# Optimization experiments

Hardware: AMD Instinct MI355X
Metric: run time of the kernel (lower is better)

## Reference

```python
import jax, jax.numpy as jnp
import numpy as np
import math

HIDDEN = 768
HEADS = 12
HEAD_DIM = HIDDEN // HEADS
B, T = 2, 2048


def setup_inputs() -> dict:
    key = jax.random.key(0)
    k1, k2, k3, k4, k5 = jax.random.split(key, 5)
    s = 0.02
    return {
        "x": jax.random.normal(k1, (B, T, HIDDEN), dtype=jnp.float32),
        "mask": jnp.ones((B, T), dtype=jnp.int32),
        "w_qkv": jax.random.normal(k2, (3 * HIDDEN, HIDDEN), dtype=jnp.float32) * s,
        "b_qkv": jnp.zeros((3 * HIDDEN,), dtype=jnp.float32),
        "w_out": jax.random.normal(k3, (HIDDEN, HIDDEN), dtype=jnp.float32) * s,
        "b_out": jnp.zeros((HIDDEN,), dtype=jnp.float32),
    }


def reference(x, mask, w_qkv, b_qkv, w_out, b_out):
    Bv, Tv, C = x.shape
    # torch Linear: y = x @ W.T + b
    qkv = jnp.einsum('btc,oc->bto', x, w_qkv) + b_qkv  # [B,T,3C]
    q, k, v = jnp.split(qkv, 3, axis=-1)
    def to_heads(t):
        return t.reshape(Bv, Tv, HEADS, HEAD_DIM).transpose(0, 2, 1, 3)  # [B,H,T,D]
    q, k, v = to_heads(q), to_heads(k), to_heads(v)
    scale = 1.0 / math.sqrt(HEAD_DIM)
    scores = jnp.einsum('bhqd,bhkd->bhqk', q, k) * scale  # [B,H,T,T]
    m = (mask[:, None, None, :] != 0)  # broadcast over heads and query dim
    scores = jnp.where(m, scores, -jnp.inf)
    probs = jax.nn.softmax(scores, axis=-1)
    # dropout is identity in eval mode
    ctx = jnp.einsum('bhqk,bhkd->bhqd', probs, v)  # [B,H,T,D]
    ctx = ctx.transpose(0, 2, 1, 3).reshape(Bv, Tv, C)
    return jnp.einsum('btc,oc->bto', ctx, w_out) + b_out
```

## Files before the change

kernel.cpp:

```cpp
#include <hip/hip_runtime.h>
#include <hip/hip_bf16.h>


typedef __bf16 bf16;
typedef __attribute__((ext_vector_type(4))) __bf16 bf16x4;
typedef __attribute__((ext_vector_type(8))) __bf16 bf16x8;
typedef __attribute__((ext_vector_type(4))) float f32x4;
typedef __attribute__((ext_vector_type(16))) float f32x16;
typedef __attribute__((ext_vector_type(4))) unsigned u32x4;

#define MFMA16(a, b, c) __builtin_amdgcn_mfma_f32_16x16x32_bf16((a), (b), (c), 0, 0, 0)
#define MFMA32(a, b, c) __builtin_amdgcn_mfma_f32_32x32x16_bf16((a), (b), (c), 0, 0, 0)

static constexpr int BB = 2;
static constexpr int TT = 2048;
static constexpr int CC = 768;
static constexpr int HH = 12;
static constexpr int DD = 64;

union U8 { u32x4 u; bf16x8 b; };

__device__ inline void gload16(const bf16* g, bf16* l) {
  __builtin_amdgcn_global_load_lds((const __attribute__((address_space(1))) void*)g,
                                   (__attribute__((address_space(3))) void*)l, 16, 0, 0);
}

__global__ __launch_bounds__(256) void cvt_all(const float* __restrict__ x,
                                               const float* __restrict__ wq,
                                               const float* __restrict__ wo,
                                               bf16* __restrict__ xb,
                                               bf16* __restrict__ wqb,
                                               bf16* __restrict__ wob) {
  const int CX = BB * TT * CC / 8, CQ = 3 * CC * CC / 8;
  int idx = blockIdx.x * 256 + threadIdx.x;
  const float* s;
  bf16* d;
  int off;
  if (idx < CX) { s = x; d = xb; off = idx; }
  else if (idx < CX + CQ) { s = wq; d = wqb; off = idx - CX; }
  else { s = wo; d = wob; off = idx - CX - CQ; }
  const float4* p = (const float4*)(s + (size_t)off * 8);
  float4 a = p[0], b = p[1];
  bf16x8 r;
  r[0] = (bf16)a.x; r[1] = (bf16)a.y; r[2] = (bf16)a.z; r[3] = (bf16)a.w;
  r[4] = (bf16)b.x; r[5] = (bf16)b.y; r[6] = (bf16)b.z; r[7] = (bf16)b.w;
  *(bf16x8*)(d + (size_t)off * 8) = r;
}

template <typename OT>
__global__ __launch_bounds__(256) void gemm_bt_bf16(const bf16* __restrict__ A,
                                                    const bf16* __restrict__ Bw,
                                                    const float* __restrict__ bias,
                                                    OT* __restrict__ Cmat,
                                                    int M, int N, int K,
                                                    float qs, int qcols) {
  __shared__ bf16 As[128 * 64];
  __shared__ bf16 Bs[128 * 64];
  const int tid = threadIdx.x;
  const int m0 = blockIdx.y * 128, n0 = blockIdx.x * 128;
  const int lane = tid & 63, w = tid >> 6;
  const int wm = (w >> 1) * 64, wn = (w & 1) * 64;
  const int lr = lane & 15;
  const int g4 = lane >> 4;
  const int srow8 = lane >> 3;
  const int scs = ((lane & 7) ^ srow8) * 8;
  f32x4 acc[4][4] = {};
  for (int k0 = 0; k0 < K; k0 += 64) {
    __syncthreads();
#pragma unroll
    for (int s = 0; s < 4; s++) {
      const int rowl = w * 32 + s * 8;
      gload16(A  + (size_t)(m0 + rowl + srow8) * K + k0 + scs, &As[rowl * 64]);
      gload16(Bw + (size_t)(n0 + rowl + srow8) * K + k0 + scs, &Bs[rowl * 64]);
    }
    __syncthreads();
#pragma unroll
    for (int ks = 0; ks < 2; ks++) {
      bf16x8 a[4], b[4];
#pragma unroll
      for (int i = 0; i < 4; i++)
        a[i] = *(const bf16x8*)&As[(wm + i * 16 + lr) * 64 + (((ks * 4 + g4) ^ (lr & 7)) * 8)];
#pragma unroll
      for (int j = 0; j < 4; j++)
        b[j] = *(const bf16x8*)&Bs[(wn + j * 16 + lr) * 64 + (((ks * 4 + g4) ^ (lr & 7)) * 8)];
#pragma unroll
      for (int i = 0; i < 4; i++)
#pragma unroll
        for (int j = 0; j < 4; j++)
          acc[i][j] = MFMA16(a[i], b[j], acc[i][j]);
    }
  }
#pragma unroll
  for (int i = 0; i < 4; i++) {
    const int rbase = m0 + wm + i * 16 + (lane >> 4) * 4;
#pragma unroll
    for (int j = 0; j < 4; j++) {
      const int cidx = n0 + wn + j * 16 + lr;
      const float bv = bias[cidx];
      const float sc = (cidx < qcols) ? qs : 1.0f;
#pragma unroll
      for (int r = 0; r < 4; r++) {
        float v = (acc[i][j][r] + bv) * sc;
        Cmat[(size_t)(rbase + r) * N + cidx] = (OT)v;
      }
    }
  }
}

template <int NS>
__global__ __launch_bounds__(256, 4) void attn_fwd(const bf16* __restrict__ qkv,
                                                   const int* __restrict__ mask,
                                                   bf16* __restrict__ po,
                                                   float* __restrict__ ml,
                                                   bf16* __restrict__ ctx) {
  __shared__ bf16 Ks[2][64 * 64];
  __shared__ bf16 Vt[2][64 * 64];
  const int tid = threadIdx.x, lane = tid & 63, w = tid >> 6;
  const int ln31 = lane & 31, hi = lane >> 5;
  const int cpx = 48 * NS;
  const int bid = blockIdx.x;
  const int wg = (bid & 7) * cpx + (bid >> 3);
  const int qb = wg & 15;
  const int t2 = wg >> 4;
  const int s = t2 % NS;
  const int bh = t2 / NS;
  const int h = bh % HH, b = bh / HH;
  const int q = qb * 128 + w * 32 + ln31;
  const size_t rs = 3 * CC;
  const float NEG = -1.0e30f;
  const int kt0 = s * (TT / NS), kt1 = kt0 + TT / NS;

  bf16x8 qreg[4];
  {
    const bf16* qp = qkv + (size_t)(b * TT + q) * rs + h * DD + hi * 8;
#pragma unroll
    for (int ds = 0; ds < 4; ds++) qreg[ds] = *(const bf16x8*)(qp + ds * 16);
  }

  const bf16* kbase = qkv + (size_t)(b * TT) * rs + CC + h * DD;
  const bf16* vbase = qkv + (size_t)(b * TT) * rs + 2 * CC + h * DD;

  const int krow = lane >> 3;
  const int klc0 = ((lane & 7) ^ (w & 7)) * 8;
  const int klc1 = ((lane & 7) ^ ((w + 4) & 7)) * 8;
  auto stage_k = [&](int buf, int kt) {
    gload16(kbase + (size_t)(kt + w * 8 + krow) * rs + klc0, &Ks[buf][(w * 8) * 64]);
    gload16(kbase + (size_t)(kt + 32 + w * 8 + krow) * rs + klc1, &Ks[buf][(32 + w * 8) * 64]);
  };

  const int vkey = tid >> 2;
  const int vd0 = (tid & 3) * 16;
  const int vpar = vkey & 1;
  const int vkp = vkey >> 1;
  bf16x8 vr0, vr1;
  int mv;
  auto load_v = [&](int kt) {
    const bf16* vp = vbase + (size_t)(kt + vkey) * rs + vd0;
    vr0 = ((const bf16x8*)vp)[0];
    vr1 = ((const bf16x8*)vp)[1];
    mv = mask[b * TT + kt + lane];
  };
  auto vt_put = [&](int buf, int d, unsigned val) {
    *(unsigned*)&Vt[buf][d * 64 + (((vkp >> 2) ^ ((d >> 3) & 7)) * 8) + (vkp & 3) * 2] = val;
  };
  auto write_v = [&](int buf) {
    U8 ua, ub; ua.b = vr0; ub.b = vr1;
    unsigned w0 = ua.u[0], w1 = ua.u[1], w2 = ua.u[2], w3 = ua.u[3];
    unsigned w4 = ub.u[0], w5 = ub.u[1], w6 = ub.u[2], w7 = ub.u[3];
    unsigned x0 = vpar ? w0 : w4, x1 = vpar ? w1 : w5;
    unsigned x2 = vpar ? w2 : w6, x3 = vpar ? w3 : w7;
    unsigned r0 = __shfl_xor(x0, 4), r1 = __shfl_xor(x1, 4);
    unsigned r2 = __shfl_xor(x2, 4), r3 = __shfl_xor(x3, 4);
    unsigned a0 = vpar ? r0 : w0, a1 = vpar ? r1 : w1;
    unsigned a2 = vpar ? r2 : w2, a3 = vpar ? r3 : w3;
    unsigned b0 = vpar ? w4 : r0, b1 = vpar ? w5 : r1;
    unsigned b2 = vpar ? w6 : r2, b3 = vpar ? w7 : r3;
    const int dbase = vd0 + vpar * 8;
    vt_put(buf, dbase + 0, (a0 & 0xffffu) | (b0 << 16));
    vt_put(buf, dbase + 1, (a0 >> 16) | (b0 & 0xffff0000u));
    vt_put(buf, dbase + 2, (a1 & 0xffffu) | (b1 << 16));
    vt_put(buf, dbase + 3, (a1 >> 16) | (b1 & 0xffff0000u));
    vt_put(buf, dbase + 4, (a2 & 0xffffu) | (b2 << 16));
    vt_put(buf, dbase + 5, (a2 >> 16) | (b2 & 0xffff0000u));
    vt_put(buf, dbase + 6, (a3 & 0xffffu) | (b3 << 16));
    vt_put(buf, dbase + 7, (a3 >> 16) | (b3 & 0xffff0000u));
  };

  stage_k(0, kt0);
  load_v(kt0);
  write_v(0);
  __syncthreads();
  int mvc = mv;

  f32x16 oacc0 = {}, oacc1 = {};
  float m = NEG, l = 0.f;
  const int rsw0 = (ln31 >> 3) & 7;
  const int rsw1 = ((32 + ln31) >> 3) & 7;

  int cur = 0;
  for (int kt = kt0; kt < kt1; kt += 64, cur ^= 1) {
    const bool more = kt + 64 < kt1;
    if (more) { stage_k(cur ^ 1, kt + 64); load_v(kt + 64); }

    f32x16 sa = {}, sb = {};
    __builtin_amdgcn_s_setprio(1);
#pragma unroll
    for (int ds = 0; ds < 4; ds++) {
      const int c0 = ds * 2 + hi;
      bf16x8 kfa = *(const bf16x8*)&Ks[cur][ln31 * 64 + ((c0 ^ rsw0) * 8)];
      sa = MFMA32(kfa, qreg[ds], sa);
      bf16x8 kfb = *(const bf16x8*)&Ks[cur][(32 + ln31) * 64 + ((c0 ^ rsw1) * 8)];
      sb = MFMA32(kfb, qreg[ds], sb);
    }
    __builtin_amdgcn_s_setprio(0);

    const unsigned long long bm = __ballot(mvc != 0);
    if (bm != ~0ull) {
#pragma unroll
      for (int r = 0; r < 16; r++) {
        const int key = (r & 3) + 8 * (r >> 2) + 4 * hi;
        if (!((bm >> key) & 1)) sa[r] = NEG;
        if (!((bm >> (key + 32)) & 1)) sb[r] = NEG;
      }
    }

    float mx = fmaxf(sa[0], sb[0]);
#pragma unroll
    for (int r = 1; r < 16; r++) mx = fmaxf(mx, fmaxf(sa[r], sb[r]));
    mx = fmaxf(mx, __shfl_xor(mx, 32));
    if (!__all(mx - m <= 8.f)) {
      const float al = exp2f(m - mx);
      l *= al;
#pragma unroll
      for (int r = 0; r < 16; r++) { oacc0[r] *= al; oacc1[r] *= al; }
      m = mx;
    }
    float rsum = 0.f;
#pragma unroll
    for (int r = 0; r < 16; r++) {
      sa[r] = exp2f(sa[r] - m); rsum += sa[r];
      sb[r] = exp2f(sb[r] - m); rsum += sb[r];
    }
    rsum += __shfl_xor(rsum, 32);
    l += rsum;

    unsigned pk[16];
#pragma unroll
    for (int i = 0; i < 8; i++) {
      asm("v_cvt_pk_bf16_f32 %0, %1, %2" : "=v"(pk[i]) : "v"(sa[2 * i]), "v"(sa[2 * i + 1]));
      asm("v_cvt_pk_bf16_f32 %0, %1, %2" : "=v"(pk[8 + i]) : "v"(sb[2 * i]), "v"(sb[2 * i + 1]));
    }
    asm volatile("v_permlane32_swap_b32 %0, %1" : "+v"(pk[0]), "+v"(pk[2]));
    asm volatile("v_permlane32_swap_b32 %0, %1" : "+v"(pk[1]), "+v"(pk[3]));
    asm volatile("v_permlane32_swap_b32 %0, %1" : "+v"(pk[4]), "+v"(pk[6]));
    asm volatile("v_permlane32_swap_b32 %0, %1" : "+v"(pk[5]), "+v"(pk[7]));
    asm volatile("v_permlane32_swap_b32 %0, %1" : "+v"(pk[8]), "+v"(pk[10]));
    asm volatile("v_permlane32_swap_b32 %0, %1" : "+v"(pk[9]), "+v"(pk[11]));
    asm volatile("v_permlane32_swap_b32 %0, %1" : "+v"(pk[12]), "+v"(pk[14]));
    asm volatile("v_permlane32_swap_b32 %0, %1" : "+v"(pk[13]), "+v"(pk[15]));

    __builtin_amdgcn_s_setprio(1);
#pragma unroll
    for (int ks = 0; ks < 4; ks++) {
      U8 uu;
      uu.u = (u32x4){pk[ks * 4 + 0], pk[ks * 4 + 1], pk[ks * 4 + 2], pk[ks * 4 + 3]};
      const bf16x8 pb = uu.b;
      const int c0 = ks * 2 + hi;
      bf16x8 vf0 = *(const bf16x8*)&Vt[cur][ln31 * 64 + ((c0 ^ rsw0) * 8)];
      oacc0 = MFMA32(vf0, pb, oacc0);
      bf16x8 vf1 = *(const bf16x8*)&Vt[cur][(32 + ln31) * 64 + ((c0 ^ rsw1) * 8)];
      oacc1 = MFMA32(vf1, pb, oacc1);
    }
    __builtin_amdgcn_s_setprio(0);

    if (more) write_v(cur ^ 1);
    __syncthreads();
    mvc = mv;
  }

  const float invl = l > 0.f ? 1.0f / l : 0.f;
  const size_t gr = (size_t)(b * TT + q);
  bf16* obase = (NS == 1) ? (ctx + gr * CC + h * DD)
                          : (po + (size_t)s * (BB * TT * CC) + gr * CC + h * DD);
#pragma unroll
  for (int g = 0; g < 4; g++) {
    bf16x4 o0, o1;
#pragma unroll
    for (int j = 0; j < 4; j++) {
      o0[j] = (bf16)(oacc0[4 * g + j] * invl);
      o1[j] = (bf16)(oacc1[4 * g + j] * invl);
    }
    *(bf16x4*)(obase + 8 * g + 4 * hi) = o0;
    *(bf16x4*)(obase + 32 + 8 * g + 4 * hi) = o1;
  }
  if (NS > 1 && hi == 0) {
    float2 v2 = {m, l};
    *(float2*)&ml[(((size_t)s * (BB * TT) + gr) * HH + h) * 2] = v2;
  }
}

template <int NS>
__global__ __launch_bounds__(256) void combine(const bf16* __restrict__ po,
                                               const float* __restrict__ ml,
                                               bf16* __restrict__ ctx) {
  const int idx = blockIdx.x * 256 + threadIdx.x;
  const int row = idx / 96;
  const int rem = idx - row * 96;
  const int h = rem >> 3, d8 = rem & 7;
  float ms[NS], ls[NS];
  float M = -1.0e30f;
#pragma unroll
  for (int s = 0; s < NS; s++) {
    const float2 p2 = *(const float2*)&ml[(((size_t)s * (BB * TT) + row) * HH + h) * 2];
    ms[s] = p2.x; ls[s] = p2.y;
    M = fmaxf(M, p2.x);
  }
  float wgt[NS], wsum = 0.f;
#pragma unroll
  for (int s = 0; s < NS; s++) { wgt[s] = ls[s] * exp2f(ms[s] - M); wsum += wgt[s]; }
  const float inv = wsum > 0.f ? 1.0f / wsum : 0.f;
  float acc[8] = {};
#pragma unroll
  for (int s = 0; s < NS; s++) {
    const float ws = wgt[s] * inv;
    const bf16x8 v = *(const bf16x8*)&po[(size_t)s * (BB * TT * CC) + (size_t)row * CC + h * 64 + d8 * 8];
#pragma unroll
    for (int j = 0; j < 8; j++) acc[j] += ws * (float)v[j];
  }
  bf16x8 o;
#pragma unroll
  for (int j = 0; j < 8; j++) o[j] = (bf16)acc[j];
  *(bf16x8*)&ctx[(size_t)row * CC + h * 64 + d8 * 8] = o;
}

extern "C" void kernel_launch(void* const* d_in, const int* in_sizes, int n_in,
                              void* d_out, int out_size, void* d_ws, size_t ws_size,
                              hipStream_t stream) {
  const float* x     = (const float*)d_in[0];
  const int*   mask  = (const int*)d_in[1];
  const float* w_qkv = (const float*)d_in[2];
  const float* b_qkv = (const float*)d_in[3];
  const float* w_out = (const float*)d_in[4];
  const float* b_out = (const float*)d_in[5];
  float* out = (float*)d_out;

  const int M = BB * TT;
  bf16* qkv = (bf16*)d_ws;
  bf16* xb  = qkv + (size_t)M * 3 * CC;
  bf16* ctx = xb;
  bf16* wob = xb + (size_t)M * CC;
  bf16* wqb = wob + (size_t)CC * CC;
  const size_t PO_OFF = (size_t)((M * 3 * CC) + (M * CC) + (CC * CC)) * 2;
  const size_t PER_SPLIT = (size_t)M * CC * 2 + (size_t)M * HH * 2 * 4;

  int NS = 1;
  if (ws_size >= PO_OFF + 4 * PER_SPLIT) NS = 4;
  else if (ws_size >= PO_OFF + 2 * PER_SPLIT) NS = 2;

  bf16* po = (bf16*)((char*)d_ws + PO_OFF);
  float* ml = (float*)((char*)d_ws + PO_OFF + (size_t)NS * M * CC * 2);

  const int nchunks = (BB * TT * CC + 3 * CC * CC + CC * CC) / 8;
  cvt_all<<<nchunks / 256, 256, 0, stream>>>(x, w_qkv, w_out, xb, wqb, wob);
  gemm_bt_bf16<bf16><<<dim3(3 * CC / 128, M / 128), 256, 0, stream>>>(
      xb, wqb, b_qkv, qkv, M, 3 * CC, CC, 0.125f * 1.44269504f, CC);
  if (NS == 4) {
    attn_fwd<4><<<dim3(384 * 4), 256, 0, stream>>>(qkv, mask, po, ml, ctx);
    combine<4><<<dim3(M * HH * 8 / 256), 256, 0, stream>>>(po, ml, ctx);
  } else if (NS == 2) {
    attn_fwd<2><<<dim3(384 * 2), 256, 0, stream>>>(qkv, mask, po, ml, ctx);
    combine<2><<<dim3(M * HH * 8 / 256), 256, 0, stream>>>(po, ml, ctx);
  } else {
    attn_fwd<1><<<dim3(384), 256, 0, stream>>>(qkv, mask, po, ml, ctx);
  }
  gemm_bt_bf16<float><<<dim3(CC / 128, M / 128), 256, 0, stream>>>(
      ctx, wob, b_out, out, M, CC, CC, 1.0f, 0);
}
```

Measured before the change: 128.7 us.

## Split softmax exp and PV MFMA into halves to overlap VALU with MFMA

```diff
diff --git a/kernel.cpp b/kernel.cpp
--- a/kernel.cpp
+++ b/kernel.cpp
@@ -108,11 +108,11 @@
 }
 
 template <int NS>
-__global__ __launch_bounds__(256, 4) void attn_fwd(const bf16* __restrict__ qkv,
-                                                   const int* __restrict__ mask,
-                                                   bf16* __restrict__ po,
-                                                   float* __restrict__ ml,
-                                                   bf16* __restrict__ ctx) {
+__global__ __launch_bounds__(256) void attn_fwd(const bf16* __restrict__ qkv,
+                                                const int* __restrict__ mask,
+                                                bf16* __restrict__ po,
+                                                float* __restrict__ ml,
+                                                bf16* __restrict__ ctx) {
   __shared__ bf16 Ks[2][64 * 64];
   __shared__ bf16 Vt[2][64 * 64];
   const int tid = threadIdx.x, lane = tid & 63, w = tid >> 6;
@@ -128,7 +128,8 @@
   const int q = qb * 128 + w * 32 + ln31;
   const size_t rs = 3 * CC;
   const float NEG = -1.0e30f;
-  const int kt0 = s * (TT / NS), kt1 = kt0 + TT / NS;
+  const int kt0 = s * (TT / NS);
+  const int NT = (TT / NS) / 64;
 
   bf16x8 qreg[4];
   {
@@ -143,23 +144,19 @@
   const int krow = lane >> 3;
   const int klc0 = ((lane & 7) ^ (w & 7)) * 8;
   const int klc1 = ((lane & 7) ^ ((w + 4) & 7)) * 8;
-  auto stage_k = [&](int buf, int kt) {
-    gload16(kbase + (size_t)(kt + w * 8 + krow) * rs + klc0, &Ks[buf][(w * 8) * 64]);
-    gload16(kbase + (size_t)(kt + 32 + w * 8 + krow) * rs + klc1, &Ks[buf][(32 + w * 8) * 64]);
-  };
+  const bf16* kptA = kbase + (size_t)(kt0 + w * 8 + krow) * rs + klc0;
+  const bf16* kptB = kbase + (size_t)(kt0 + 32 + w * 8 + krow) * rs + klc1;
 
   const int vkey = tid >> 2;
   const int vd0 = (tid & 3) * 16;
   const int vpar = vkey & 1;
   const int vkp = vkey >> 1;
+  const bf16* vptr = vbase + (size_t)(kt0 + vkey) * rs + vd0;
+  const int* mptr = mask + b * TT + kt0 + lane;
+  const size_t stride = (size_t)64 * rs;
+
   bf16x8 vr0, vr1;
   int mv;
-  auto load_v = [&](int kt) {
-    const bf16* vp = vbase + (size_t)(kt + vkey) * rs + vd0;
-    vr0 = ((const bf16x8*)vp)[0];
-    vr1 = ((const bf16x8*)vp)[1];
-    mv = mask[b * TT + kt + lane];
-  };
   auto vt_put = [&](int buf, int d, unsigned val) {
     *(unsigned*)&Vt[buf][d * 64 + (((vkp >> 2) ^ ((d >> 3) & 7)) * 8) + (vkp & 3) * 2] = val;
   };
@@ -186,9 +183,13 @@
     vt_put(buf, dbase + 7, (a3 >> 16) | (b3 & 0xffff0000u));
   };
 
-  stage_k(0, kt0);
-  load_v(kt0);
+  gload16(kptA, &Ks[0][(w * 8) * 64]);
+  gload16(kptB, &Ks[0][(32 + w * 8) * 64]);
+  vr0 = ((const bf16x8*)vptr)[0];
+  vr1 = ((const bf16x8*)vptr)[1];
+  mv = *mptr;
   write_v(0);
+  kptA += stride; kptB += stride; vptr += stride; mptr += 64;
   __syncthreads();
   int mvc = mv;
 
@@ -198,9 +199,16 @@
   const int rsw1 = ((32 + ln31) >> 3) & 7;
 
   int cur = 0;
-  for (int kt = kt0; kt < kt1; kt += 64, cur ^= 1) {
-    const bool more = kt + 64 < kt1;
-    if (more) { stage_k(cur ^ 1, kt + 64); load_v(kt + 64); }
+  for (int it = 0; it < NT; ++it, cur ^= 1) {
+    const bool more = (it + 1 < NT);
+    if (more) {
+      gload16(kptA, &Ks[cur ^ 1][(w * 8) * 64]);
+      gload16(kptB, &Ks[cur ^ 1][(32 + w * 8) * 64]);
+      vr0 = ((const bf16x8*)vptr)[0];
+      vr1 = ((const bf16x8*)vptr)[1];
+      mv = *mptr;
+      kptA += stride; kptB += stride; vptr += stride; mptr += 64;
+    }
 
     f32x16 sa = {}, sb = {};
     __builtin_amdgcn_s_setprio(1);
@@ -224,9 +232,12 @@
       }
     }
 
-    float mx = fmaxf(sa[0], sb[0]);
-#pragma unroll
-    for (int r = 1; r < 16; r++) mx = fmaxf(mx, fmaxf(sa[r], sb[r]));
+    float t[8];
+#pragma unroll
+    for (int i = 0; i < 8; i++)
+      t[i] = fmaxf(fmaxf(sa[2 * i], sa[2 * i + 1]), fmaxf(sb[2 * i], sb[2 * i + 1]));
+    float mx = fmaxf(fmaxf(fmaxf(t[0], t[1]), fmaxf(t[2], t[3])),
+                     fmaxf(fmaxf(t[4], t[5]), fmaxf(t[6], t[7])));
     mx = fmaxf(mx, __shfl_xor(mx, 32));
     if (!__all(mx - m <= 8.f)) {
       const float al = exp2f(m - mx);
@@ -235,43 +246,55 @@
       for (int r = 0; r < 16; r++) { oacc0[r] *= al; oacc1[r] *= al; }
       m = mx;
     }
+
     float rsum = 0.f;
-#pragma unroll
-    for (int r = 0; r < 16; r++) {
-      sa[r] = exp2f(sa[r] - m); rsum += sa[r];
-      sb[r] = exp2f(sb[r] - m); rsum += sb[r];
-    }
-    rsum += __shfl_xor(rsum, 32);
-    l += rsum;
-
-    unsigned pk[16];
-#pragma unroll
-    for (int i = 0; i < 8; i++) {
+    unsigned pk[8];
+#pragma unroll
+    for (int r = 0; r < 16; r++) { sa[r] = exp2f(sa[r] - m); rsum += sa[r]; }
+#pragma unroll
+    for (int i = 0; i < 8; i++)
       asm("v_cvt_pk_bf16_f32 %0, %1, %2" : "=v"(pk[i]) : "v"(sa[2 * i]), "v"(sa[2 * i + 1]));
-      asm("v_cvt_pk_bf16_f32 %0, %1, %2" : "=v"(pk[8 + i]) : "v"(sb[2 * i]), "v"(sb[2 * i + 1]));
-    }
     asm volatile("v_permlane32_swap_b32 %0, %1" : "+v"(pk[0]), "+v"(pk[2]));
     asm volatile("v_permlane32_swap_b32 %0, %1" : "+v"(pk[1]), "+v"(pk[3]));
     asm volatile("v_permlane32_swap_b32 %0, %1" : "+v"(pk[4]), "+v"(pk[6]));
     asm volatile("v_permlane32_swap_b32 %0, %1" : "+v"(pk[5]), "+v"(pk[7]));
-    asm volatile("v_permlane32_swap_b32 %0, %1" : "+v"(pk[8]), "+v"(pk[10]));
-    asm volatile("v_permlane32_swap_b32 %0, %1" : "+v"(pk[9]), "+v"(pk[11]));
-    asm volatile("v_permlane32_swap_b32 %0, %1" : "+v"(pk[12]), "+v"(pk[14]));
-    asm volatile("v_permlane32_swap_b32 %0, %1" : "+v"(pk[13]), "+v"(pk[15]));
-
     __builtin_amdgcn_s_setprio(1);
 #pragma unroll
-    for (int ks = 0; ks < 4; ks++) {
+    for (int ks = 0; ks < 2; ks++) {
       U8 uu;
       uu.u = (u32x4){pk[ks * 4 + 0], pk[ks * 4 + 1], pk[ks * 4 + 2], pk[ks * 4 + 3]};
-      const bf16x8 pb = uu.b;
       const int c0 = ks * 2 + hi;
       bf16x8 vf0 = *(const bf16x8*)&Vt[cur][ln31 * 64 + ((c0 ^ rsw0) * 8)];
-      oacc0 = MFMA32(vf0, pb, oacc0);
+      oacc0 = MFMA32(vf0, uu.b, oacc0);
       bf16x8 vf1 = *(const bf16x8*)&Vt[cur][(32 + ln31) * 64 + ((c0 ^ rsw1) * 8)];
-      oacc1 = MFMA32(vf1, pb, oacc1);
+      oacc1 = MFMA32(vf1, uu.b, oacc1);
     }
     __builtin_amdgcn_s_setprio(0);
+#pragma unroll
+    for (int r = 0; r < 16; r++) { sb[r] = exp2f(sb[r] - m); rsum += sb[r]; }
+#pragma unroll
+    for (int i = 0; i < 8; i++)
+      asm("v_cvt_pk_bf16_f32 %0, %1, %2" : "=v"(pk[i]) : "v"(sb[2 * i]), "v"(sb[2 * i + 1]));
+    asm volatile("v_permlane32_swap_b32 %0, %1" : "+v"(pk[0]), "+v"(pk[2]));
+    asm volatile("v_permlane32_swap_b32 %0, %1" : "+v"(pk[1]), "+v"(pk[3]));
+    asm volatile("v_permlane32_swap_b32 %0, %1" : "+v"(pk[4]), "+v"(pk[6]));
+    asm volatile("v_permlane32_swap_b32 %0, %1" : "+v"(pk[5]), "+v"(pk[7]));
+    __builtin_amdgcn_s_setprio(1);
+#pragma unroll
+    for (int ks = 2; ks < 4; ks++) {
+      U8 uu;
+      uu.u = (u32x4){pk[(ks - 2) * 4 + 0], pk[(ks - 2) * 4 + 1],
+                     pk[(ks - 2) * 4 + 2], pk[(ks - 2) * 4 + 3]};
+      const int c0 = ks * 2 + hi;
+      bf16x8 vf0 = *(const bf16x8*)&Vt[cur][ln31 * 64 + ((c0 ^ rsw0) * 8)];
+      oacc0 = MFMA32(vf0, uu.b, oacc0);
+      bf16x8 vf1 = *(const bf16x8*)&Vt[cur][(32 + ln31) * 64 + ((c0 ^ rsw1) * 8)];
+      oacc1 = MFMA32(vf1, uu.b, oacc1);
+    }
+    __builtin_amdgcn_s_setprio(0);
+
+    rsum += __shfl_xor(rsum, 32);
+    l += rsum;
 
     if (more) write_v(cur ^ 1);
     __syncthreads();
```

Result: faster. 123.7 us (-3.9%).
